# Optimization experiments

Hardware: AMD Instinct MI355X
Metric: run time of the kernel (lower is better)

Reference implementation:

```python
import jax, jax.numpy as jnp
import numpy as np

NUM_TREES = 100
TREE_DEPTH = 5
INPUT_DIM = 256
NUM_CLASSES = 64
BATCH = 8192
NUM_NODES = 2 ** TREE_DEPTH - 1   # 31 decision nodes per tree
NUM_LEAVES = 2 ** TREE_DEPTH      # 32 leaves per tree


def setup_inputs() -> dict:
    key = jax.random.key(0)
    k_x, k_w, k_b, k_l = jax.random.split(key, 4)
    x = jax.random.normal(k_x, (BATCH, INPUT_DIM), dtype=jnp.float32)
    # stacked per-tree decision-node params (torch.randn init)
    node_w = jax.random.normal(k_w, (NUM_TREES, NUM_NODES, INPUT_DIM), dtype=jnp.float32)
    node_b = jax.random.normal(k_b, (NUM_TREES, NUM_NODES), dtype=jnp.float32)
    leaves = jax.random.normal(k_l, (NUM_TREES, NUM_LEAVES, NUM_CLASSES), dtype=jnp.float32)
    return {"x": x, "node_w": node_w, "node_b": node_b, "leaves": leaves}


def reference(x, node_w, node_b, leaves):
    # x: [B, D]; node_w: [T, Nn, D]; node_b: [T, Nn]; leaves: [T, Nl, C]
    T = node_w.shape[0]
    B = x.shape[0]
    depth = int(np.log2(leaves.shape[1]))
    idx = jnp.zeros((T, B), dtype=jnp.int32)
    for _ in range(depth):  # small fixed depth loop
        # gather each sample's routing node per tree: [T, B, D] and [T, B]
        w_g = jnp.take_along_axis(node_w, idx[:, :, None], axis=1)
        b_g = jnp.take_along_axis(node_b, idx, axis=1)
        decisions = jax.nn.sigmoid(jnp.einsum('tbd,bd->tb', w_g, x) + b_g)
        idx = 2 * idx + (decisions <= 0.5).astype(jnp.int32)
    # leaf gather: [T, B, C], then forest average over trees -> [B, C]
    tree_preds = jnp.take_along_axis(leaves, idx[:, :, None], axis=1)
    return jnp.mean(tree_preds, axis=0)
```

## Files before the change

kernel.cpp:

```cpp
#include <hip/hip_runtime.h>


typedef __bf16 bf16;
typedef __attribute__((ext_vector_type(8))) __bf16 bf16x8;
typedef __attribute__((ext_vector_type(4))) float f32x4;

#define NTREES 100
#define NB     8192
#define ND     256
#define NNODES 31
#define NLEAF  32
#define NCLS   64
#define TAU    2.0e-3f
#define QCAP   8192

static __device__ __forceinline__ void gload16(const void* g, void* l) {
    __builtin_amdgcn_global_load_lds(
        (const __attribute__((address_space(1))) void*)g,
        (__attribute__((address_space(3))) void*)l, 16, 0, 0);
}

__global__ void prep(const float* __restrict__ x, const float* __restrict__ wf,
                     const float* __restrict__ lv,
                     bf16* __restrict__ xh, bf16* __restrict__ xl,
                     bf16* __restrict__ wimg, bf16* __restrict__ lv16,
                     unsigned int* __restrict__ qcount) {
    if (blockIdx.x == 0 && threadIdx.x == 0) *qcount = 0;
    if (blockIdx.x < 1024) {
        int i = blockIdx.x * 256 + threadIdx.x;
        int m  = i & 15;
        int dq = (i >> 4) & 31;
        int g  = i >> 9;
        const float* src = x + (size_t)(g * 16 + m) * ND + dq * 8;
        bf16x8 h8, l8;
#pragma unroll
        for (int e = 0; e < 8; ++e) {
            float f = src[e];
            bf16 h = (bf16)f;
            h8[e] = h;
            l8[e] = (bf16)(f - (float)h);
        }
        *(bf16x8*)(xh + (size_t)i * 8) = h8;
        *(bf16x8*)(xl + (size_t)i * 8) = l8;
    } else if (blockIdx.x < 1224) {
        int i = (blockIdx.x - 1024) * 256 + threadIdx.x;
        int oct = i & 31;
        int row = (i >> 5) & 63;
        int tg  = i >> 11;
        int tree = tg * 4 + (row >> 4), node = row & 15;
        const float* src = wf + ((size_t)tree * NNODES + node) * ND + oct * 8;
        bf16x8 h8, l8;
#pragma unroll
        for (int e = 0; e < 8; ++e) {
            float f = src[e];
            bf16 h = (bf16)f;
            h8[e] = h;
            l8[e] = (bf16)(f - (float)h);
        }
        int kc = oct >> 4, c = oct & 15, cp = c ^ (row & 7);
        size_t b = (size_t)tg * 32768 + (size_t)kc * 16384 + row * 128 + cp * 8;
        *(bf16x8*)(wimg + b)        = h8;
        *(bf16x8*)(wimg + b + 8192) = l8;
    } else {
        int i = (blockIdx.x - 1224) * 256 + threadIdx.x;
        lv16[i] = (bf16)lv[i];
    }
}

__global__ __launch_bounds__(256, 3) void forest_all(
    const bf16* __restrict__ xh, const bf16* __restrict__ xl,
    const bf16* __restrict__ wimg,
    const float* __restrict__ bias,
    unsigned char* __restrict__ idxb,
    unsigned int* __restrict__ qcount, unsigned int* __restrict__ queue)
{
    __shared__ char lds[32768];
    bf16*  Wh  = (bf16*)lds;
    bf16*  Wl  = (bf16*)(lds + 16384);
    float* scr = (float*)lds;

    const int tid  = threadIdx.x;
    const int wave = tid >> 6;
    const int lane = tid & 63;
    const int m    = lane & 15;
    const int q    = lane >> 4;

    const int lin  = blockIdx.x + gridDim.x * blockIdx.y;
    const int xcd  = lin & 7;
    const int slot = lin >> 3;
    const int mg   = xcd * 4 + (slot / 25);
    const int tg   = slot % 25;

    float biasv[4];
#pragma unroll
    for (int ni = 0; ni < 4; ++ni)
        biasv[ni] = bias[(size_t)(tg * 4 + ni) * NNODES + m];

    f32x4 acc[4][4];
#pragma unroll
    for (int mi = 0; mi < 4; ++mi)
#pragma unroll
        for (int ni = 0; ni < 4; ++ni)
            acc[mi][ni] = (f32x4){0.f, 0.f, 0.f, 0.f};

    size_t abase[4];
#pragma unroll
    for (int mi = 0; mi < 4; ++mi)
        abase[mi] = (size_t)(mg * 16 + wave * 4 + mi) * 4096 + lane * 8;

    const bf16* wsrc = wimg + (size_t)tg * 32768;

    bf16x8 cah[4], cal[4], nah[4], nal[4];
#pragma unroll
    for (int mi = 0; mi < 4; ++mi) {
        cah[mi] = *(const bf16x8*)(xh + abase[mi]);
        cal[mi] = *(const bf16x8*)(xl + abase[mi]);
    }

#pragma unroll
    for (int kc = 0; kc < 2; ++kc) {
        __syncthreads();
#pragma unroll
        for (int j = 0; j < 8; ++j) {
            int idx = j * 256 + tid;
            gload16(wsrc + (size_t)kc * 16384 + idx * 8, lds + idx * 16);
        }
        __syncthreads();

#pragma unroll
        for (int kk = 0; kk < 4; ++kk) {
            if (kk < 3 || kc == 0) {
                size_t step = (kk < 3) ? (size_t)(kc * 16 + (kk + 1) * 4) * 128
                                       : (size_t)(16) * 128;
#pragma unroll
                for (int mi = 0; mi < 4; ++mi) {
                    nah[mi] = *(const bf16x8*)(xh + abase[mi] + step);
                    nal[mi] = *(const bf16x8*)(xl + abase[mi] + step);
                }
            }
#pragma unroll
            for (int ni = 0; ni < 4; ++ni) {
                const int n    = ni * 16 + m;
                const int cidx = (4 * kk + q) ^ (m & 7);
                bf16x8 bh = *(const bf16x8*)(Wh + n * 128 + cidx * 8);
                bf16x8 bl = *(const bf16x8*)(Wl + n * 128 + cidx * 8);
#pragma unroll
                for (int mi = 0; mi < 4; ++mi) {
                    acc[mi][ni] = __builtin_amdgcn_mfma_f32_16x16x32_bf16(cal[mi], bh, acc[mi][ni], 0, 0, 0);
                    acc[mi][ni] = __builtin_amdgcn_mfma_f32_16x16x32_bf16(cah[mi], bl, acc[mi][ni], 0, 0, 0);
                    acc[mi][ni] = __builtin_amdgcn_mfma_f32_16x16x32_bf16(cah[mi], bh, acc[mi][ni], 0, 0, 0);
                }
            }
#pragma unroll
            for (int mi = 0; mi < 4; ++mi) { cah[mi] = nah[mi]; cal[mi] = nal[mi]; }
        }
    }
    __syncthreads();

    float* ws_ = scr + wave * 1280;
    const int s_l = wave * 64 + lane;
    const int sg  = mg * 256 + s_l;
    unsigned int pk = 0;
#pragma unroll
    for (int ni = 0; ni < 4; ++ni) {
#pragma unroll
        for (int mi = 0; mi < 4; ++mi)
#pragma unroll
            for (int r = 0; r < 4; ++r)
                ws_[(mi * 16 + q * 4 + r) * 20 + m] = acc[mi][ni][r] + biasv[ni];
        f32x4 z0 = *(f32x4*)&ws_[lane * 20];
        f32x4 z1 = *(f32x4*)&ws_[lane * 20 + 4];
        f32x4 z2 = *(f32x4*)&ws_[lane * 20 + 8];
        f32x4 z3 = *(f32x4*)&ws_[lane * 20 + 12];
        float z[16] = {z0[0], z0[1], z0[2], z0[3], z1[0], z1[1], z1[2], z1[3],
                       z2[0], z2[1], z2[2], z2[3], z3[0], z3[1], z3[2], z3[3]};
        float a0 = z[0];
        bool d0 = a0 <= 0.f;
        float a1 = d0 ? z[1] : z[0];
        bool d1 = a1 <= 0.f;
        float a2 = d0 ? (d1 ? z[3] : z[2]) : (d1 ? z[1] : z[0]);
        bool d2 = a2 <= 0.f;
        float m0 = d2 ? z[1] : z[0], m1 = d2 ? z[3] : z[2];
        float m2 = d2 ? z[5] : z[4], m3 = d2 ? z[7] : z[6];
        float p0 = d1 ? m1 : m0, p1 = d1 ? m3 : m2;
        float a3 = d0 ? p1 : p0;
        bool d3 = a3 <= 0.f;
        float n0 = d3 ? z[1] : z[0],  n1 = d3 ? z[3] : z[2];
        float n2 = d3 ? z[5] : z[4],  n3 = d3 ? z[7] : z[6];
        float n4 = d3 ? z[9] : z[8],  n5 = d3 ? z[11] : z[10];
        float n6 = d3 ? z[13] : z[12], n7 = d3 ? z[15] : z[14];
        float q0 = d2 ? n1 : n0, q1 = d2 ? n3 : n2;
        float q2 = d2 ? n5 : n4, q3 = d2 ? n7 : n6;
        float r0 = d1 ? q1 : q0, r1 = d1 ? q3 : q2;
        float a4 = d0 ? r1 : r0;
        bool d4 = a4 <= 0.f;
        int leaf = ((int)d0 << 4) | ((int)d1 << 3) | ((int)d2 << 2)
                 | ((int)d3 << 1) | (int)d4;
        pk |= (unsigned)leaf << (8 * ni);
        float mn = fminf(fminf(fminf(fabsf(a0), fabsf(a1)),
                               fminf(fabsf(a2), fabsf(a3))), fabsf(a4));
        if (mn < TAU) {
            unsigned int pos = atomicAdd(qcount, 1u);
            if (pos < QCAP)
                queue[pos] = ((unsigned)(tg * 4 + ni) << 13) | (unsigned)sg;
        }
        __syncthreads();
    }
    *(unsigned int*)(idxb + (size_t)sg * NTREES + tg * 4) = pk;
}

__global__ void fixup_kernel(const float* __restrict__ x, const float* __restrict__ wf,
                             const float* __restrict__ bias,
                             const unsigned int* __restrict__ qcount,
                             const unsigned int* __restrict__ queue,
                             unsigned char* __restrict__ idxb) {
    const int wid  = (blockIdx.x * 256 + threadIdx.x) >> 6;
    const int lane = threadIdx.x & 63;
    unsigned int n = *qcount;
    if (n > QCAP) n = QCAP;
    for (unsigned int it = wid; it < n; it += 256) {
        unsigned int e = queue[it];
        int t = e >> 13, s = e & 8191;
        const float* xr = x + (size_t)s * ND;
        float4 xv = *(const float4*)(xr + lane * 4);
        int node = 0;
        for (int lvl = 0; lvl < 5; ++lvl) {
            const float* wr = wf + ((size_t)t * NNODES + node) * ND;
            float4 wv = *(const float4*)(wr + lane * 4);
            double zz = (double)xv.x * wv.x + (double)xv.y * wv.y
                      + (double)xv.z * wv.z + (double)xv.w * wv.w;
#pragma unroll
            for (int o = 32; o > 0; o >>= 1) zz += __shfl_xor(zz, o);
            zz += (double)bias[t * NNODES + node];
            node = 2 * node + (zz <= 0.0 ? 1 : 0);
        }
        if (lane == 0) idxb[(size_t)s * NTREES + t] = (unsigned char)node;
    }
}

__global__ void leaf_gather(const unsigned char* __restrict__ idxb,
                            const bf16* __restrict__ lv16,
                            float* __restrict__ out) {
    const int wave = threadIdx.x >> 6;
    const int lane = threadIdx.x & 63;
    const int s = blockIdx.x * 4 + wave;
    unsigned int rw = 0;
    if (lane < 25) rw = *(const unsigned int*)(idxb + (size_t)s * NTREES + lane * 4);
    float acc = 0.f;
#pragma unroll 10
    for (int t = 0; t < NTREES; ++t) {
        unsigned int wrd = __shfl(rw, t >> 2);
        int li = (wrd >> ((t & 3) * 8)) & 255;
        acc += (float)lv16[((size_t)t * NLEAF + li) * NCLS + lane];
    }
    out[(size_t)s * NCLS + lane] = acc * 0.01f;
}

extern "C" void kernel_launch(void* const* d_in, const int* in_sizes, int n_in,
                              void* d_out, int out_size, void* d_ws, size_t ws_size,
                              hipStream_t stream) {
    const float* x  = (const float*)d_in[0];
    const float* nw = (const float*)d_in[1];
    const float* nb = (const float*)d_in[2];
    const float* lv = (const float*)d_in[3];
    float* out = (float*)d_out;

    char* ws = (char*)d_ws;
    bf16* xh   = (bf16*)(ws + 0);
    bf16* xl   = (bf16*)(ws + 4194304);
    bf16* wimg = (bf16*)(ws + 8388608);
    unsigned char* idxb = (unsigned char*)(ws + 10027008);
    bf16* lv16 = (bf16*)(ws + 10846208);
    unsigned int* qcount = (unsigned int*)(ws + 11255808);
    unsigned int* queue  = (unsigned int*)(ws + 11255824);
    if (ws_size < (size_t)11288592) return;

    prep<<<2024, 256, 0, stream>>>(x, nw, lv, xh, xl, wimg, lv16, qcount);
    forest_all<<<dim3(25, 32), 256, 0, stream>>>(
        xh, xl, wimg, nb, idxb, qcount, queue);
    fixup_kernel<<<64, 256, 0, stream>>>(x, nw, nb, qcount, queue, idxb);
    leaf_gather<<<NB / 4, 256, 0, stream>>>(idxb, lv16, out);
}
```

Baseline: 110.2 us.

## Widen tree tile to 8 trees per block with double-buffered K-quarter weight loads

```diff
diff --git a/kernel.cpp b/kernel.cpp
--- a/kernel.cpp
+++ b/kernel.cpp
@@ -42,41 +42,44 @@
         }
         *(bf16x8*)(xh + (size_t)i * 8) = h8;
         *(bf16x8*)(xl + (size_t)i * 8) = l8;
-    } else if (blockIdx.x < 1224) {
+    } else if (blockIdx.x < 1232) {
         int i = (blockIdx.x - 1024) * 256 + threadIdx.x;
-        int oct = i & 31;
-        int row = (i >> 5) & 63;
-        int tg  = i >> 11;
-        int tree = tg * 4 + (row >> 4), node = row & 15;
-        const float* src = wf + ((size_t)tree * NNODES + node) * ND + oct * 8;
+        int oct_g = i & 31;
+        int row   = (i >> 5) & 127;
+        int tg    = i >> 12;
+        int tree  = tg * 8 + (row >> 4), node = row & 15;
         bf16x8 h8, l8;
-#pragma unroll
-        for (int e = 0; e < 8; ++e) {
-            float f = src[e];
-            bf16 h = (bf16)f;
-            h8[e] = h;
-            l8[e] = (bf16)(f - (float)h);
-        }
-        int kc = oct >> 4, c = oct & 15, cp = c ^ (row & 7);
-        size_t b = (size_t)tg * 32768 + (size_t)kc * 16384 + row * 128 + cp * 8;
+        if (tree < NTREES) {
+            const float* src = wf + ((size_t)tree * NNODES + node) * ND + oct_g * 8;
+#pragma unroll
+            for (int e = 0; e < 8; ++e) {
+                float f = src[e];
+                bf16 h = (bf16)f;
+                h8[e] = h;
+                l8[e] = (bf16)(f - (float)h);
+            }
+        } else {
+#pragma unroll
+            for (int e = 0; e < 8; ++e) { h8[e] = (bf16)0.f; l8[e] = (bf16)0.f; }
+        }
+        int kq = oct_g >> 3, oct = oct_g & 7, cp = oct ^ (row & 7);
+        size_t b = (size_t)tg * 65536 + (size_t)kq * 16384 + row * 64 + cp * 8;
         *(bf16x8*)(wimg + b)        = h8;
         *(bf16x8*)(wimg + b + 8192) = l8;
     } else {
-        int i = (blockIdx.x - 1224) * 256 + threadIdx.x;
+        int i = (blockIdx.x - 1232) * 256 + threadIdx.x;
         lv16[i] = (bf16)lv[i];
     }
 }
 
-__global__ __launch_bounds__(256, 3) void forest_all(
+__global__ __launch_bounds__(256, 2) void forest_all(
     const bf16* __restrict__ xh, const bf16* __restrict__ xl,
     const bf16* __restrict__ wimg,
     const float* __restrict__ bias,
     unsigned char* __restrict__ idxb,
     unsigned int* __restrict__ qcount, unsigned int* __restrict__ queue)
 {
-    __shared__ char lds[32768];
-    bf16*  Wh  = (bf16*)lds;
-    bf16*  Wl  = (bf16*)(lds + 16384);
+    __shared__ char lds[65536];
     float* scr = (float*)lds;
 
     const int tid  = threadIdx.x;
@@ -88,19 +91,21 @@
     const int lin  = blockIdx.x + gridDim.x * blockIdx.y;
     const int xcd  = lin & 7;
     const int slot = lin >> 3;
-    const int mg   = xcd * 4 + (slot / 25);
-    const int tg   = slot % 25;
-
-    float biasv[4];
-#pragma unroll
-    for (int ni = 0; ni < 4; ++ni)
-        biasv[ni] = bias[(size_t)(tg * 4 + ni) * NNODES + m];
-
-    f32x4 acc[4][4];
+    const int mg   = xcd * 4 + (slot / 13);
+    const int tg   = slot % 13;
+
+    float biasv[8];
+#pragma unroll
+    for (int ni = 0; ni < 8; ++ni) {
+        int tree = tg * 8 + ni;
+        biasv[ni] = (tree < NTREES) ? bias[(size_t)tree * NNODES + m] : 0.f;
+    }
+
+    f32x4 acc[4][8];
 #pragma unroll
     for (int mi = 0; mi < 4; ++mi)
 #pragma unroll
-        for (int ni = 0; ni < 4; ++ni)
+        for (int ni = 0; ni < 8; ++ni)
             acc[mi][ni] = (f32x4){0.f, 0.f, 0.f, 0.f};
 
     size_t abase[4];
@@ -108,7 +113,14 @@
     for (int mi = 0; mi < 4; ++mi)
         abase[mi] = (size_t)(mg * 16 + wave * 4 + mi) * 4096 + lane * 8;
 
-    const bf16* wsrc = wimg + (size_t)tg * 32768;
+    const bf16* wsrc = wimg + (size_t)tg * 65536;
+
+#pragma unroll
+    for (int j = 0; j < 8; ++j) {
+        int idx = j * 256 + tid;
+        gload16(wsrc + idx * 8, lds + idx * 16);
+    }
+    __syncthreads();
 
     bf16x8 cah[4], cal[4], nah[4], nal[4];
 #pragma unroll
@@ -118,32 +130,32 @@
     }
 
 #pragma unroll
-    for (int kc = 0; kc < 2; ++kc) {
-        __syncthreads();
-#pragma unroll
-        for (int j = 0; j < 8; ++j) {
-            int idx = j * 256 + tid;
-            gload16(wsrc + (size_t)kc * 16384 + idx * 8, lds + idx * 16);
-        }
-        __syncthreads();
-
-#pragma unroll
-        for (int kk = 0; kk < 4; ++kk) {
-            if (kk < 3 || kc == 0) {
-                size_t step = (kk < 3) ? (size_t)(kc * 16 + (kk + 1) * 4) * 128
-                                       : (size_t)(16) * 128;
+    for (int kq = 0; kq < 4; ++kq) {
+        const char* bufc = lds + (kq & 1) * 32768;
+        if (kq < 3) {
+            char* bufn = lds + ((kq + 1) & 1) * 32768;
+#pragma unroll
+            for (int j = 0; j < 8; ++j) {
+                int idx = j * 256 + tid;
+                gload16(wsrc + (size_t)(kq + 1) * 16384 + idx * 8, bufn + idx * 16);
+            }
+        }
+#pragma unroll
+        for (int kkq = 0; kkq < 2; ++kkq) {
+            const int kk = kq * 2 + kkq;
+            if (kk < 7) {
 #pragma unroll
                 for (int mi = 0; mi < 4; ++mi) {
-                    nah[mi] = *(const bf16x8*)(xh + abase[mi] + step);
-                    nal[mi] = *(const bf16x8*)(xl + abase[mi] + step);
+                    nah[mi] = *(const bf16x8*)(xh + abase[mi] + (kk + 1) * 512);
+                    nal[mi] = *(const bf16x8*)(xl + abase[mi] + (kk + 1) * 512);
                 }
             }
 #pragma unroll
-            for (int ni = 0; ni < 4; ++ni) {
-                const int n    = ni * 16 + m;
-                const int cidx = (4 * kk + q) ^ (m & 7);
-                bf16x8 bh = *(const bf16x8*)(Wh + n * 128 + cidx * 8);
-                bf16x8 bl = *(const bf16x8*)(Wl + n * 128 + cidx * 8);
+            for (int ni = 0; ni < 8; ++ni) {
+                const int n  = ni * 16 + m;
+                const int cp = (kkq * 4 + q) ^ (m & 7);
+                bf16x8 bh = *(const bf16x8*)((const bf16*)bufc + n * 64 + cp * 8);
+                bf16x8 bl = *(const bf16x8*)((const bf16*)bufc + 8192 + n * 64 + cp * 8);
 #pragma unroll
                 for (int mi = 0; mi < 4; ++mi) {
                     acc[mi][ni] = __builtin_amdgcn_mfma_f32_16x16x32_bf16(cal[mi], bh, acc[mi][ni], 0, 0, 0);
@@ -154,15 +166,15 @@
 #pragma unroll
             for (int mi = 0; mi < 4; ++mi) { cah[mi] = nah[mi]; cal[mi] = nal[mi]; }
         }
-    }
-    __syncthreads();
+        __syncthreads();
+    }
 
     float* ws_ = scr + wave * 1280;
     const int s_l = wave * 64 + lane;
     const int sg  = mg * 256 + s_l;
-    unsigned int pk = 0;
-#pragma unroll
-    for (int ni = 0; ni < 4; ++ni) {
+    unsigned int pk0 = 0, pk1 = 0;
+#pragma unroll
+    for (int ni = 0; ni < 8; ++ni) {
 #pragma unroll
         for (int mi = 0; mi < 4; ++mi)
 #pragma unroll
@@ -196,17 +208,20 @@
         bool d4 = a4 <= 0.f;
         int leaf = ((int)d0 << 4) | ((int)d1 << 3) | ((int)d2 << 2)
                  | ((int)d3 << 1) | (int)d4;
-        pk |= (unsigned)leaf << (8 * ni);
+        if (ni < 4) pk0 |= (unsigned)leaf << (8 * ni);
+        else        pk1 |= (unsigned)leaf << (8 * (ni - 4));
         float mn = fminf(fminf(fminf(fabsf(a0), fabsf(a1)),
                                fminf(fabsf(a2), fabsf(a3))), fabsf(a4));
-        if (mn < TAU) {
+        const int tree = tg * 8 + ni;
+        if (tree < NTREES && mn < TAU) {
             unsigned int pos = atomicAdd(qcount, 1u);
             if (pos < QCAP)
-                queue[pos] = ((unsigned)(tg * 4 + ni) << 13) | (unsigned)sg;
-        }
-        __syncthreads();
-    }
-    *(unsigned int*)(idxb + (size_t)sg * NTREES + tg * 4) = pk;
+                queue[pos] = ((unsigned)tree << 13) | (unsigned)sg;
+        }
+    }
+    unsigned char* dst = idxb + (size_t)sg * NTREES + tg * 8;
+    *(unsigned int*)dst = pk0;
+    if (tg < 12) *(unsigned int*)(dst + 4) = pk1;
 }
 
 __global__ void fixup_kernel(const float* __restrict__ x, const float* __restrict__ wf,
@@ -269,14 +284,14 @@
     bf16* xh   = (bf16*)(ws + 0);
     bf16* xl   = (bf16*)(ws + 4194304);
     bf16* wimg = (bf16*)(ws + 8388608);
-    unsigned char* idxb = (unsigned char*)(ws + 10027008);
-    bf16* lv16 = (bf16*)(ws + 10846208);
-    unsigned int* qcount = (unsigned int*)(ws + 11255808);
-    unsigned int* queue  = (unsigned int*)(ws + 11255824);
-    if (ws_size < (size_t)11288592) return;
-
-    prep<<<2024, 256, 0, stream>>>(x, nw, lv, xh, xl, wimg, lv16, qcount);
-    forest_all<<<dim3(25, 32), 256, 0, stream>>>(
+    unsigned char* idxb = (unsigned char*)(ws + 10092544);
+    bf16* lv16 = (bf16*)(ws + 10911744);
+    unsigned int* qcount = (unsigned int*)(ws + 11321344);
+    unsigned int* queue  = (unsigned int*)(ws + 11321360);
+    if (ws_size < (size_t)11354128) return;
+
+    prep<<<2032, 256, 0, stream>>>(x, nw, lv, xh, xl, wimg, lv16, qcount);
+    forest_all<<<dim3(13, 32), 256, 0, stream>>>(
         xh, xl, wimg, nb, idxb, qcount, queue);
     fixup_kernel<<<64, 256, 0, stream>>>(x, nw, nb, qcount, queue, idxb);
     leaf_gather<<<NB / 4, 256, 0, stream>>>(idxb, lv16, out);
```

Result: no change. 109.2 us (median of 2 runs) (-1.0%).
